# Performance work log

Measured on AMD Instinct MI355X. Metric: run time of the kernel, lower is better.

Reference implementation:

```python
import jax, jax.numpy as jnp
import numpy as np

N = 100000
E = 1600000
HID = 128
TEMB = 128
NH = 4
NG = 16
LN_EPS = 1e-5


def setup_inputs() -> dict:
    key = jax.random.key(0)
    ks = jax.random.split(key, 12)
    x = jax.random.normal(ks[0], (N, HID + 2), dtype=jnp.float32)
    edge_index = jax.random.randint(ks[1], (2, E), 0, N, dtype=jnp.int64)
    edge_attr = jax.random.normal(ks[2], (E, HID), dtype=jnp.float32)
    u = jax.random.normal(ks[3], (NG, TEMB), dtype=jnp.float32)
    batch = jax.random.randint(ks[4], (N,), 0, NG, dtype=jnp.int64)
    in_dim = HID * 2 + NH + TEMB  # 388
    s = 0.05
    W_proj = jax.random.normal(ks[5], (HID, NH * 2), dtype=jnp.float32) * s
    b_proj = jnp.zeros((NH * 2,), dtype=jnp.float32)
    W1 = jax.random.normal(ks[6], (in_dim, HID), dtype=jnp.float32) * s
    b1 = jnp.zeros((HID,), dtype=jnp.float32)
    ln_g = jnp.ones((HID,), dtype=jnp.float32)
    ln_b = jnp.zeros((HID,), dtype=jnp.float32)
    W2 = jax.random.normal(ks[7], (HID, HID), dtype=jnp.float32) * s
    b2 = jnp.zeros((HID,), dtype=jnp.float32)
    return {"x": x, "edge_index": edge_index, "edge_attr": edge_attr, "u": u,
            "batch": batch, "W_proj": W_proj, "b_proj": b_proj, "W1": W1,
            "b1": b1, "ln_g": ln_g, "ln_b": ln_b, "W2": W2, "b2": b2}


def reference(x, edge_index, edge_attr, u, batch, W_proj, b_proj, W1, b1, ln_g, ln_b, W2, b2):
    row, col = edge_index[0], edge_index[1]
    h_E = x[:, :-2]                     # [N, HID]
    pos = x[:, -2:]                     # [N, 2]
    delta = pos[col] - pos[row]         # [E, 2]
    dx = delta[:, 0:1]
    dy = delta[:, 1:2]
    Hv = (edge_attr @ W_proj + b_proj).reshape(-1, NH, 2)  # [E, NH, 2]
    C_ij = Hv[:, :, 0] * (-dy) + Hv[:, :, 1] * dx          # [E, NH]
    n = x.shape[0]
    phys_curl = jax.ops.segment_sum(C_ij, col, num_segments=n)     # [N, NH]
    m_i = jax.ops.segment_sum(edge_attr, col, num_segments=n)      # [N, HID]
    tau = u[batch]                                                 # [N, TEMB]
    node_in = jnp.concatenate([h_E, m_i, phys_curl, tau], axis=-1)  # [N, 388]
    h = node_in @ W1 + b1
    mu = jnp.mean(h, axis=-1, keepdims=True)
    var = jnp.var(h, axis=-1, keepdims=True)
    h = (h - mu) * jax.lax.rsqrt(var + LN_EPS) * ln_g + ln_b
    h = h * jax.nn.sigmoid(h)  # SiLU
    return h @ W2 + b2
```

## Files before the change

kernel.cpp:

```cpp
#include <hip/hip_runtime.h>
#include <hip/hip_bf16.h>

#define N_NODES 100000
#define E_EDGES 1600000
#define HID 128
#define LN_EPS 1e-5f
#define SCAN_CHUNK 1024
#define NB_SCAN ((N_NODES + SCAN_CHUNK - 1) / SCAN_CHUNK)

typedef __attribute__((ext_vector_type(4))) float f32x4;

__global__ __launch_bounds__(256)
void k_hist(const int* __restrict__ eidx, int* __restrict__ deg) {
    int e = blockIdx.x * 256 + threadIdx.x;
    if (e < E_EDGES) atomicAdd(&deg[eidx[E_EDGES + e]], 1);
}

__global__ __launch_bounds__(256)
void k_scan1(const int* __restrict__ deg, int* __restrict__ bsum) {
    __shared__ int s[256];
    int b = blockIdx.x, t = threadIdx.x;
    int sum = 0;
#pragma unroll
    for (int i = 0; i < 4; ++i) {
        int idx = b * SCAN_CHUNK + i * 256 + t;
        sum += (idx < N_NODES) ? deg[idx] : 0;
    }
    s[t] = sum; __syncthreads();
    for (int off = 128; off > 0; off >>= 1) {
        if (t < off) s[t] += s[t + off];
        __syncthreads();
    }
    if (t == 0) bsum[b] = s[0];
}

__global__ __launch_bounds__(256)
void k_scan2(int* __restrict__ bsum, int* __restrict__ offsets) {
    __shared__ int s[256];
    int t = threadIdx.x;
    int v = (t < NB_SCAN) ? bsum[t] : 0;
    s[t] = v; __syncthreads();
    for (int off = 1; off < 256; off <<= 1) {
        int add = (t >= off) ? s[t - off] : 0;
        __syncthreads();
        s[t] += add;
        __syncthreads();
    }
    if (t < NB_SCAN) bsum[t] = s[t] - v;
    if (t == NB_SCAN - 1) offsets[N_NODES] = s[t];
}

__global__ __launch_bounds__(256)
void k_scan3(const int* __restrict__ deg, const int* __restrict__ bsum,
             int* __restrict__ offsets) {
    __shared__ int s[256];
    int b = blockIdx.x, t = threadIdx.x;
    int base = b * SCAN_CHUNK + t * 4;
    int v[4]; int sum = 0;
#pragma unroll
    for (int i = 0; i < 4; ++i) {
        v[i] = (base + i < N_NODES) ? deg[base + i] : 0;
        sum += v[i];
    }
    s[t] = sum; __syncthreads();
    for (int off = 1; off < 256; off <<= 1) {
        int add = (t >= off) ? s[t - off] : 0;
        __syncthreads();
        s[t] += add;
        __syncthreads();
    }
    int toff = bsum[b] + s[t] - sum;
#pragma unroll
    for (int i = 0; i < 4; ++i) {
        if (base + i < N_NODES) offsets[base + i] = toff;
        toff += v[i];
    }
}

__global__ __launch_bounds__(256)
void k_fill(const int* __restrict__ eidx, const int* __restrict__ offsets,
            int* __restrict__ cursor, int* __restrict__ elist) {
    int e = blockIdx.x * 256 + threadIdx.x;
    if (e >= E_EDGES) return;
    int c = eidx[E_EDGES + e];
    int pos = atomicAdd(&cursor[c], 1);
    elist[offsets[c] + pos] = e;
}

__global__ __launch_bounds__(256)
void k_gather(const float* __restrict__ x,
              const int* __restrict__ eidx,
              const float* __restrict__ edge_attr,
              const float* __restrict__ W_proj,
              const float* __restrict__ b_proj,
              const int* __restrict__ offsets,
              const int* __restrict__ elist,
              float* m_i,
              float* __restrict__ curl)
{
    __shared__ float Wp[HID * 8];
    for (int i = threadIdx.x; i < HID * 8; i += 256) Wp[i] = W_proj[i];
    __syncthreads();

    int wave = threadIdx.x >> 6;
    int lane = threadIdx.x & 63;
    int c = blockIdx.x * 4 + wave;
    if (c >= N_NODES) return;

    float pcx = x[(size_t)c * 130 + 128];
    float pcy = x[(size_t)c * 130 + 129];

    int jb = offsets[c];
    int cnt = offsets[c + 1] - jb;

    float m0 = 0, m1 = 0, p0 = 0, p1 = 0, q0 = 0, q1 = 0, sdx = 0, sdy = 0;

    float2 aC = make_float2(0, 0), aN = make_float2(0, 0);
    float dxC = 0, dyC = 0, dxN = 0, dyN = 0;

    if (cnt > 0) {
        int e = elist[jb]; int r = eidx[e];
        dxC = pcx - x[(size_t)r * 130 + 128];
        dyC = pcy - x[(size_t)r * 130 + 129];
        aC = *(const float2*)(edge_attr + (size_t)e * HID + lane * 2);
    }
    if (cnt > 1) {
        int e = elist[jb + 1]; int r = eidx[e];
        dxN = pcx - x[(size_t)r * 130 + 128];
        dyN = pcy - x[(size_t)r * 130 + 129];
        aN = *(const float2*)(edge_attr + (size_t)e * HID + lane * 2);
    }

    for (int j = 0; j < cnt; ++j) {
        float2 a = aC; float dx = dxC, dy = dyC;
        aC = aN; dxC = dxN; dyC = dyN;
        if (j + 2 < cnt) {
            int e = elist[jb + j + 2]; int r = eidx[e];
            dxN = pcx - x[(size_t)r * 130 + 128];
            dyN = pcy - x[(size_t)r * 130 + 129];
            aN = *(const float2*)(edge_attr + (size_t)e * HID + lane * 2);
        }
        m0 += a.x;      m1 += a.y;
        p0 += a.x * dx; p1 += a.y * dx;
        q0 -= a.x * dy; q1 -= a.y * dy;
        sdx += dx;      sdy += dy;
    }

    *(float2*)(m_i + (size_t)c * HID + lane * 2) = make_float2(m0, m1);

    const float* w0 = &Wp[(2 * lane) * 8];
    const float* w1 = &Wp[(2 * lane + 1) * 8];
    float part[4];
#pragma unroll
    for (int h = 0; h < 4; ++h)
        part[h] = q0 * w0[2 * h] + p0 * w0[2 * h + 1] + q1 * w1[2 * h] + p1 * w1[2 * h + 1];
#pragma unroll
    for (int m = 1; m < 64; m <<= 1)
#pragma unroll
        for (int h = 0; h < 4; ++h) part[h] += __shfl_xor(part[h], m);

    if (lane == 0) {
#pragma unroll
        for (int h = 0; h < 4; ++h)
            curl[(size_t)c * 4 + h] = part[h] - b_proj[2 * h] * sdy + b_proj[2 * h + 1] * sdx;
    }
}

__global__ __launch_bounds__(256)
void node_valu(const float* __restrict__ x,
               const float* m_i,
               const float* __restrict__ curl,
               const float* __restrict__ u,
               const int* __restrict__ batch,
               const float* __restrict__ W1,
               const float* __restrict__ b1,
               const float* __restrict__ ln_g, const float* __restrict__ ln_b,
               const float* __restrict__ W2,
               const float* __restrict__ b2,
               float* out)
{
    __shared__ float Af[32 * 396];
    __shared__ float2 pss[32][2];
    __shared__ float curl_s[32 * 4];

    const int tid = threadIdx.x;
    const int base = blockIdx.x * 32;

    for (int idx = tid; idx < 32 * 64; idx += 256) {
        int n = idx >> 6, g = idx & 63;
        int node = base + n;
        float2 v = make_float2(0.f, 0.f);
        if (node < N_NODES) v = *(const float2*)(x + (size_t)node * 130 + g * 2);
        *(float2*)&Af[n * 396 + g * 2] = v;
    }
    for (int idx = tid; idx < 32 * 32; idx += 256) {
        int n = idx >> 5, g = idx & 31;
        int node = base + n;
        float4 v = make_float4(0.f, 0.f, 0.f, 0.f);
        if (node < N_NODES) v = *(const float4*)(m_i + (size_t)node * 128 + g * 4);
        *(float4*)&Af[n * 396 + 128 + g * 4] = v;
    }
    for (int idx = tid; idx < 32 * 32; idx += 256) {
        int n = idx >> 5, g = idx & 31;
        int node = base + n;
        float4 v = make_float4(0.f, 0.f, 0.f, 0.f);
        if (node < N_NODES) v = *(const float4*)(u + (size_t)batch[node] * 128 + g * 4);
        *(float4*)&Af[n * 396 + 256 + g * 4] = v;
    }
    for (int idx = tid; idx < 32 * 4; idx += 256) {
        int node = base + (idx >> 2);
        curl_s[idx] = (node < N_NODES) ? curl[(size_t)node * 4 + (idx & 3)] : 0.f;
    }
    __syncthreads();

    const int lane = tid & 63;
    const int wave = tid >> 6;
    const int band = wave >> 1;
    const int fh   = wave & 1;
    const int cg = lane >> 4, cl = lane & 15;
    const int nl0  = band * 16 + cg * 4;

    const float* a0 = &Af[(nl0 + 0) * 396];
    const float* a1 = &Af[(nl0 + 1) * 396];
    const float* a2 = &Af[(nl0 + 2) * 396];
    const float* a3 = &Af[(nl0 + 3) * 396];

    f32x4 acc[4];
#pragma unroll
    for (int f = 0; f < 4; ++f) {
        int col = (fh * 4 + f) * 16 + cl;
        float s0 = 0.f, s1 = 0.f, s2 = 0.f, s3 = 0.f;
        for (int k = 0; k < 256; ++k) {
            float w = W1[(size_t)k * 128 + col];
            s0 += a0[k] * w; s1 += a1[k] * w; s2 += a2[k] * w; s3 += a3[k] * w;
        }
        for (int k = 256; k < 384; ++k) {
            float w = W1[(size_t)(k + 4) * 128 + col];
            s0 += a0[k] * w; s1 += a1[k] * w; s2 += a2[k] * w; s3 += a3[k] * w;
        }
        acc[f] = (f32x4){s0, s1, s2, s3};
    }

#pragma unroll
    for (int f = 0; f < 4; ++f) {
        int col = (fh * 4 + f) * 16 + cl;
        float w0 = W1[(size_t)256 * 128 + col];
        float w1 = W1[(size_t)257 * 128 + col];
        float w2 = W1[(size_t)258 * 128 + col];
        float w3 = W1[(size_t)259 * 128 + col];
        float bb = b1[col];
#pragma unroll
        for (int r = 0; r < 4; ++r) {
            const float* cs = &curl_s[(nl0 + r) * 4];
            acc[f][r] += bb + cs[0] * w0 + cs[1] * w1 + cs[2] * w2 + cs[3] * w3;
        }
    }

    float sA[4], ssA[4];
#pragma unroll
    for (int r = 0; r < 4; ++r) {
        float s = 0.f, ss = 0.f;
#pragma unroll
        for (int f = 0; f < 4; ++f) { float h = acc[f][r]; s += h; ss += h * h; }
#pragma unroll
        for (int m = 1; m < 16; m <<= 1) {
            s  += __shfl_xor(s, m);
            ss += __shfl_xor(ss, m);
        }
        sA[r] = s; ssA[r] = ss;
    }
    if (cl == 0) {
#pragma unroll
        for (int r = 0; r < 4; ++r) pss[nl0 + r][fh] = make_float2(sA[r], ssA[r]);
    }
    __syncthreads();

    float gvv[4], bvv[4];
#pragma unroll
    for (int f = 0; f < 4; ++f) {
        int col = (fh * 4 + f) * 16 + cl;
        gvv[f] = ln_g[col]; bvv[f] = ln_b[col];
    }

#pragma unroll
    for (int r = 0; r < 4; ++r) {
        float2 p0 = pss[nl0 + r][0], p1 = pss[nl0 + r][1];
        float s = p0.x + p1.x, ss = p0.y + p1.y;
        float mu  = s * (1.f / 128.f);
        float var = ss * (1.f / 128.f) - mu * mu;
        float inv = rsqrtf(var + LN_EPS);
#pragma unroll
        for (int f = 0; f < 4; ++f) {
            float h = (acc[f][r] - mu) * inv * gvv[f] + bvv[f];
            h = h / (1.f + expf(-h));
            Af[(nl0 + r) * 396 + (fh * 4 + f) * 16 + cl] = h;
        }
    }
    __syncthreads();

    f32x4 acc2[4];
#pragma unroll
    for (int f = 0; f < 4; ++f) {
        int col = (fh * 4 + f) * 16 + cl;
        float s0 = 0.f, s1 = 0.f, s2 = 0.f, s3 = 0.f;
        for (int k2 = 0; k2 < 128; ++k2) {
            float w = W2[(size_t)k2 * 128 + col];
            s0 += a0[k2] * w; s1 += a1[k2] * w; s2 += a2[k2] * w; s3 += a3[k2] * w;
        }
        acc2[f] = (f32x4){s0, s1, s2, s3};
    }

#pragma unroll
    for (int f = 0; f < 4; ++f) {
        int col = (fh * 4 + f) * 16 + cl;
        float bb = b2[col];
#pragma unroll
        for (int r = 0; r < 4; ++r) {
            int node = base + nl0 + r;
            if (node < N_NODES) out[(size_t)node * 128 + col] = acc2[f][r] + bb;
        }
    }
}

extern "C" void kernel_launch(void* const* d_in, const int* in_sizes, int n_in,
                              void* d_out, int out_size, void* d_ws, size_t ws_size,
                              hipStream_t stream) {
    const float* x         = (const float*)d_in[0];
    const int*   eidx      = (const int*)d_in[1];
    const float* edge_attr = (const float*)d_in[2];
    const float* u         = (const float*)d_in[3];
    const int*   batch     = (const int*)d_in[4];
    const float* W_proj    = (const float*)d_in[5];
    const float* b_proj    = (const float*)d_in[6];
    const float* W1        = (const float*)d_in[7];
    const float* b1        = (const float*)d_in[8];
    const float* ln_g      = (const float*)d_in[9];
    const float* ln_b      = (const float*)d_in[10];
    const float* W2        = (const float*)d_in[11];
    const float* b2        = (const float*)d_in[12];

    float* out = (float*)d_out;

    char* p = (char*)d_ws;
    size_t off = 0;
    auto take = [&](size_t bytes) {
        char* q = p + off;
        off += (bytes + 255) & ~(size_t)255;
        return q;
    };
    (void)take(49152 * 2);
    (void)take(49152 * 2);
    (void)take(16384 * 2);
    (void)take(16384 * 2);
    int* deg     = (int*)take(N_NODES * 4);
    int* cursor  = (int*)take(N_NODES * 4);
    int* offsets = (int*)take((N_NODES + 1) * 4);
    int* bsum    = (int*)take(256 * 4);
    int* elist   = (int*)take((size_t)E_EDGES * 4);
    float* curl  = (float*)take((size_t)N_NODES * 4 * 4);

    hipMemsetAsync(deg, 0, (size_t)N_NODES * 4, stream);
    hipMemsetAsync(cursor, 0, (size_t)N_NODES * 4, stream);

    k_hist <<<(E_EDGES + 255) / 256, 256, 0, stream>>>(eidx, deg);
    k_scan1<<<NB_SCAN, 256, 0, stream>>>(deg, bsum);
    k_scan2<<<1, 256, 0, stream>>>(bsum, offsets);
    k_scan3<<<NB_SCAN, 256, 0, stream>>>(deg, bsum, offsets);
    k_fill <<<(E_EDGES + 255) / 256, 256, 0, stream>>>(eidx, offsets, cursor, elist);

    k_gather<<<(N_NODES + 3) / 4, 256, 0, stream>>>(
        x, eidx, edge_attr, W_proj, b_proj, offsets, elist, out, curl);

    node_valu<<<(N_NODES + 31) / 32, 256, 0, stream>>>(
        x, out, curl, u, batch, W1, b1, ln_g, ln_b, W2, b2, out);
}
```

Baseline: 968.0 us.

## Compute second node GEMM with bf16 MFMA using split-precision W2

```diff
diff --git a/kernel.cpp b/kernel.cpp
--- a/kernel.cpp
+++ b/kernel.cpp
@@ -8,7 +8,18 @@
 #define SCAN_CHUNK 1024
 #define NB_SCAN ((N_NODES + SCAN_CHUNK - 1) / SCAN_CHUNK)
 
+typedef __attribute__((ext_vector_type(8))) __bf16 bf16x8;
 typedef __attribute__((ext_vector_type(4))) float f32x4;
+typedef __attribute__((ext_vector_type(8))) unsigned short u16x8;
+
+__device__ __forceinline__ unsigned short f2bf(float v) {
+    __hip_bfloat16 h = __float2bfloat16(v);
+    return __builtin_bit_cast(unsigned short, h);
+}
+__device__ __forceinline__ float bf2f(unsigned short us) {
+    unsigned int v = ((unsigned int)us) << 16;
+    return __builtin_bit_cast(float, v);
+}
 
 __global__ __launch_bounds__(256)
 void k_hist(const int* __restrict__ eidx, int* __restrict__ deg) {
@@ -85,6 +96,23 @@
     int c = eidx[E_EDGES + e];
     int pos = atomicAdd(&cursor[c], 1);
     elist[offsets[c] + pos] = e;
+}
+
+__global__ __launch_bounds__(256)
+void k_prep2(const float* __restrict__ W2,
+             unsigned short* __restrict__ W2ph, unsigned short* __restrict__ W2pl)
+{
+    int t = blockIdx.x * 256 + threadIdx.x;
+    if (t < 4 * 8 * 64 * 8) {
+        int j = t & 7, l = (t >> 3) & 63;
+        int rest = t >> 9;
+        int f = rest & 7, kc = rest >> 3;
+        int k = kc * 32 + (l >> 4) * 8 + j;
+        float w = W2[(size_t)k * 128 + f * 16 + (l & 15)];
+        unsigned short h = f2bf(w);
+        W2ph[t] = h;
+        W2pl[t] = f2bf(w - bf2f(h));
+    }
 }
 
 __global__ __launch_bounds__(256)
@@ -167,19 +195,21 @@
 }
 
 __global__ __launch_bounds__(256)
-void node_valu(const float* __restrict__ x,
-               const float* m_i,
-               const float* __restrict__ curl,
-               const float* __restrict__ u,
-               const int* __restrict__ batch,
-               const float* __restrict__ W1,
-               const float* __restrict__ b1,
-               const float* __restrict__ ln_g, const float* __restrict__ ln_b,
-               const float* __restrict__ W2,
-               const float* __restrict__ b2,
-               float* out)
+void node_hyb(const float* __restrict__ x,
+              const float* m_i,
+              const float* __restrict__ curl,
+              const float* __restrict__ u,
+              const int* __restrict__ batch,
+              const float* __restrict__ W1,
+              const float* __restrict__ b1,
+              const float* __restrict__ ln_g, const float* __restrict__ ln_b,
+              const unsigned short* __restrict__ W2ph,
+              const unsigned short* __restrict__ W2pl,
+              const float* __restrict__ b2,
+              float* out)
 {
     __shared__ float Af[32 * 396];
+    __shared__ unsigned short Sm[32 * 136];
     __shared__ float2 pss[32][2];
     __shared__ float curl_s[32 * 4];
 
@@ -218,6 +248,7 @@
     const int band = wave >> 1;
     const int fh   = wave & 1;
     const int cg = lane >> 4, cl = lane & 15;
+    const int rowA = band * 16 + cl;
     const int nl0  = band * 16 + cg * 4;
 
     const float* a0 = &Af[(nl0 + 0) * 396];
@@ -293,21 +324,27 @@
         for (int f = 0; f < 4; ++f) {
             float h = (acc[f][r] - mu) * inv * gvv[f] + bvv[f];
             h = h / (1.f + expf(-h));
-            Af[(nl0 + r) * 396 + (fh * 4 + f) * 16 + cl] = h;
+            Sm[(nl0 + r) * 136 + (fh * 4 + f) * 16 + cl] = f2bf(h);
         }
     }
     __syncthreads();
 
     f32x4 acc2[4];
 #pragma unroll
-    for (int f = 0; f < 4; ++f) {
-        int col = (fh * 4 + f) * 16 + cl;
-        float s0 = 0.f, s1 = 0.f, s2 = 0.f, s3 = 0.f;
-        for (int k2 = 0; k2 < 128; ++k2) {
-            float w = W2[(size_t)k2 * 128 + col];
-            s0 += a0[k2] * w; s1 += a1[k2] * w; s2 += a2[k2] * w; s3 += a3[k2] * w;
-        }
-        acc2[f] = (f32x4){s0, s1, s2, s3};
+    for (int f = 0; f < 4; ++f) acc2[f] = (f32x4){0.f, 0.f, 0.f, 0.f};
+
+#pragma unroll
+    for (int kc = 0; kc < 4; ++kc) {
+        u16x8 araw = *(const u16x8*)&Sm[rowA * 136 + kc * 32 + cg * 8];
+        bf16x8 AS = __builtin_bit_cast(bf16x8, araw);
+#pragma unroll
+        for (int f = 0; f < 4; ++f) {
+            size_t fo = ((size_t)(kc * 8 + fh * 4 + f) * 64 + lane) * 8;
+            bf16x8 BH = __builtin_bit_cast(bf16x8, *(const u16x8*)(W2ph + fo));
+            bf16x8 BL = __builtin_bit_cast(bf16x8, *(const u16x8*)(W2pl + fo));
+            acc2[f] = __builtin_amdgcn_mfma_f32_16x16x32_bf16(AS, BH, acc2[f], 0, 0, 0);
+            acc2[f] = __builtin_amdgcn_mfma_f32_16x16x32_bf16(AS, BL, acc2[f], 0, 0, 0);
+        }
     }
 
 #pragma unroll
@@ -350,8 +387,8 @@
     };
     (void)take(49152 * 2);
     (void)take(49152 * 2);
-    (void)take(16384 * 2);
-    (void)take(16384 * 2);
+    unsigned short* W2ph = (unsigned short*)take(16384 * 2);
+    unsigned short* W2pl = (unsigned short*)take(16384 * 2);
     int* deg     = (int*)take(N_NODES * 4);
     int* cursor  = (int*)take(N_NODES * 4);
     int* offsets = (int*)take((N_NODES + 1) * 4);
@@ -362,6 +399,7 @@
     hipMemsetAsync(deg, 0, (size_t)N_NODES * 4, stream);
     hipMemsetAsync(cursor, 0, (size_t)N_NODES * 4, stream);
 
+    k_prep2<<<64, 256, 0, stream>>>(W2, W2ph, W2pl);
     k_hist <<<(E_EDGES + 255) / 256, 256, 0, stream>>>(eidx, deg);
     k_scan1<<<NB_SCAN, 256, 0, stream>>>(deg, bsum);
     k_scan2<<<1, 256, 0, stream>>>(bsum, offsets);
@@ -371,6 +409,6 @@
     k_gather<<<(N_NODES + 3) / 4, 256, 0, stream>>>(
         x, eidx, edge_attr, W_proj, b_proj, offsets, elist, out, curl);
 
-    node_valu<<<(N_NODES + 31) / 32, 256, 0, stream>>>(
-        x, out, curl, u, batch, W1, b1, ln_g, ln_b, W2, b2, out);
-}
+    node_hyb<<<(N_NODES + 31) / 32, 256, 0, stream>>>(
+        x, out, curl, u, batch, W1, b1, ln_g, ln_b, W2ph, W2pl, b2, out);
+}
```

Measured after the change: 974.5 us. No clear change (+0.7%).

## Precompute per-edge position deltas in CSR fill and stream them in gather

Applied to the files above, without the earlier changes.

```diff
diff --git a/kernel.cpp b/kernel.cpp
--- a/kernel.cpp
+++ b/kernel.cpp
@@ -14,6 +14,13 @@
 void k_hist(const int* __restrict__ eidx, int* __restrict__ deg) {
     int e = blockIdx.x * 256 + threadIdx.x;
     if (e < E_EDGES) atomicAdd(&deg[eidx[E_EDGES + e]], 1);
+}
+
+__global__ __launch_bounds__(256)
+void k_pos(const float* __restrict__ x, float2* __restrict__ pos2) {
+    int c = blockIdx.x * 256 + threadIdx.x;
+    if (c < N_NODES)
+        pos2[c] = make_float2(x[(size_t)c * 130 + 128], x[(size_t)c * 130 + 129]);
 }
 
 __global__ __launch_bounds__(256)
@@ -79,17 +86,22 @@
 
 __global__ __launch_bounds__(256)
 void k_fill(const int* __restrict__ eidx, const int* __restrict__ offsets,
-            int* __restrict__ cursor, int* __restrict__ elist) {
+            const float2* __restrict__ pos2,
+            int* __restrict__ cursor, int* __restrict__ elist,
+            float2* __restrict__ dxy) {
     int e = blockIdx.x * 256 + threadIdx.x;
     if (e >= E_EDGES) return;
     int c = eidx[E_EDGES + e];
+    int r = eidx[e];
     int pos = atomicAdd(&cursor[c], 1);
-    elist[offsets[c] + pos] = e;
-}
-
-__global__ __launch_bounds__(256)
-void k_gather(const float* __restrict__ x,
-              const int* __restrict__ eidx,
+    int slot = offsets[c] + pos;
+    elist[slot] = e;
+    float2 pc = pos2[c], pr = pos2[r];
+    dxy[slot] = make_float2(pc.x - pr.x, pc.y - pr.y);
+}
+
+__global__ __launch_bounds__(256)
+void k_gather(const float2* __restrict__ dxy,
               const float* __restrict__ edge_attr,
               const float* __restrict__ W_proj,
               const float* __restrict__ b_proj,
@@ -107,43 +119,37 @@
     int c = blockIdx.x * 4 + wave;
     if (c >= N_NODES) return;
 
-    float pcx = x[(size_t)c * 130 + 128];
-    float pcy = x[(size_t)c * 130 + 129];
-
     int jb = offsets[c];
     int cnt = offsets[c + 1] - jb;
 
     float m0 = 0, m1 = 0, p0 = 0, p1 = 0, q0 = 0, q1 = 0, sdx = 0, sdy = 0;
 
     float2 aC = make_float2(0, 0), aN = make_float2(0, 0);
-    float dxC = 0, dyC = 0, dxN = 0, dyN = 0;
+    float2 dC = make_float2(0, 0), dN = make_float2(0, 0);
 
     if (cnt > 0) {
-        int e = elist[jb]; int r = eidx[e];
-        dxC = pcx - x[(size_t)r * 130 + 128];
-        dyC = pcy - x[(size_t)r * 130 + 129];
+        int e = elist[jb];
+        dC = dxy[jb];
         aC = *(const float2*)(edge_attr + (size_t)e * HID + lane * 2);
     }
     if (cnt > 1) {
-        int e = elist[jb + 1]; int r = eidx[e];
-        dxN = pcx - x[(size_t)r * 130 + 128];
-        dyN = pcy - x[(size_t)r * 130 + 129];
+        int e = elist[jb + 1];
+        dN = dxy[jb + 1];
         aN = *(const float2*)(edge_attr + (size_t)e * HID + lane * 2);
     }
 
     for (int j = 0; j < cnt; ++j) {
-        float2 a = aC; float dx = dxC, dy = dyC;
-        aC = aN; dxC = dxN; dyC = dyN;
+        float2 a = aC; float2 d = dC;
+        aC = aN; dC = dN;
         if (j + 2 < cnt) {
-            int e = elist[jb + j + 2]; int r = eidx[e];
-            dxN = pcx - x[(size_t)r * 130 + 128];
-            dyN = pcy - x[(size_t)r * 130 + 129];
+            int e = elist[jb + j + 2];
+            dN = dxy[jb + j + 2];
             aN = *(const float2*)(edge_attr + (size_t)e * HID + lane * 2);
         }
-        m0 += a.x;      m1 += a.y;
-        p0 += a.x * dx; p1 += a.y * dx;
-        q0 -= a.x * dy; q1 -= a.y * dy;
-        sdx += dx;      sdy += dy;
+        m0 += a.x;       m1 += a.y;
+        p0 += a.x * d.x; p1 += a.y * d.x;
+        q0 -= a.x * d.y; q1 -= a.y * d.y;
+        sdx += d.x;      sdy += d.y;
     }
 
     *(float2*)(m_i + (size_t)c * HID + lane * 2) = make_float2(m0, m1);
@@ -358,18 +364,21 @@
     int* bsum    = (int*)take(256 * 4);
     int* elist   = (int*)take((size_t)E_EDGES * 4);
     float* curl  = (float*)take((size_t)N_NODES * 4 * 4);
+    float2* pos2 = (float2*)take((size_t)N_NODES * 8);
+    float2* dxy  = (float2*)take((size_t)E_EDGES * 8);
 
     hipMemsetAsync(deg, 0, (size_t)N_NODES * 4, stream);
     hipMemsetAsync(cursor, 0, (size_t)N_NODES * 4, stream);
 
+    k_pos  <<<(N_NODES + 255) / 256, 256, 0, stream>>>(x, pos2);
     k_hist <<<(E_EDGES + 255) / 256, 256, 0, stream>>>(eidx, deg);
     k_scan1<<<NB_SCAN, 256, 0, stream>>>(deg, bsum);
     k_scan2<<<1, 256, 0, stream>>>(bsum, offsets);
     k_scan3<<<NB_SCAN, 256, 0, stream>>>(deg, bsum, offsets);
-    k_fill <<<(E_EDGES + 255) / 256, 256, 0, stream>>>(eidx, offsets, cursor, elist);
+    k_fill <<<(E_EDGES + 255) / 256, 256, 0, stream>>>(eidx, offsets, pos2, cursor, elist, dxy);
 
     k_gather<<<(N_NODES + 3) / 4, 256, 0, stream>>>(
-        x, eidx, edge_attr, W_proj, b_proj, offsets, elist, out, curl);
+        dxy, edge_attr, W_proj, b_proj, offsets, elist, out, curl);
 
     node_valu<<<(N_NODES + 31) / 32, 256, 0, stream>>>(
         x, out, curl, u, batch, W1, b1, ln_g, ln_b, W2, b2, out);
```

Measured after the change: 886.4 us. -8.4%, faster.
